# Optimization experiments

Measured on AMD Instinct MI355X. Metric: run time of the kernel, lower is better.

## Reference

```python
import jax, jax.numpy as jnp
import numpy as np

HEADS = 16
DIM_HEAD = 64
DIM = 1024
INNER = HEADS * DIM_HEAD  # 1024


def setup_inputs() -> dict:
    key = jax.random.key(0)
    ks = jax.random.split(key, 8)
    B, N, M = 4, 2048, 2048
    x = jax.random.normal(ks[0], (B, N, DIM), dtype=jnp.float32)
    context = jax.random.normal(ks[1], (B, M, DIM), dtype=jnp.float32)
    x_mask = (jax.random.uniform(ks[2], (B, N)) > 0.1).astype(jnp.float32)
    context_mask = (jax.random.uniform(ks[3], (B, M)) > 0.1).astype(jnp.float32)
    s = 0.02
    Wq = jax.random.normal(ks[4], (DIM, INNER), dtype=jnp.float32) * s
    Wkv = jax.random.normal(ks[5], (DIM, 2 * INNER), dtype=jnp.float32) * s
    Wo = jax.random.normal(ks[6], (INNER, DIM), dtype=jnp.float32) * s
    bo = jnp.zeros((DIM,), dtype=jnp.float32)
    return {"x": x, "context": context, "x_mask": x_mask,
            "context_mask": context_mask, "Wq": Wq, "Wkv": Wkv, "Wo": Wo, "bo": bo}


def _split_heads(t):
    b, n, _ = t.shape
    return t.reshape(b, n, HEADS, DIM_HEAD).transpose(0, 2, 1, 3)  # b h n d


def reference(x, context, x_mask, context_mask, Wq, Wkv, Wo, bo):
    scale = DIM_HEAD ** -0.5
    q = _split_heads(x @ Wq)                       # b h n d
    kv = context @ Wkv
    k = _split_heads(kv[..., :INNER])              # b h m d
    v = _split_heads(kv[..., INNER:])              # b h m d
    dots = jnp.einsum('bhnd,bhmd->bhnm', q, k) * scale
    # attn_bias = 1 - x_mask ⊗ context_mask; masked where isclose(attn_bias, 1)
    prod = x_mask[:, None, :, None] * context_mask[:, None, None, :]  # b 1 n m
    masked = jnp.isclose(1.0 - prod, 1.0)          # b 1 n m, broadcast over heads
    dots = jnp.where(masked, -jnp.inf, dots)       # b h n m
    # rows with no valid key: zero the whole row before softmax
    valid = jnp.any(~masked, axis=-1, keepdims=True)  # b 1 n 1
    dots = jnp.where(valid, dots, 0.0)
    attn = jax.nn.softmax(dots, axis=-1)
    attn = jnp.where(valid, attn, 0.0)
    out = jnp.einsum('bhnm,bhmd->bhnd', attn, v)
    b, h, n, d = out.shape
    out = out.transpose(0, 2, 1, 3).reshape(b, n, h * d)
    return out @ Wo + bo
```

## Files before the change

### kernel.cpp

```cpp
#include <hip/hip_runtime.h>

#define DEVI __device__ __forceinline__

typedef __attribute__((ext_vector_type(4))) float f32x4;
typedef __attribute__((ext_vector_type(8))) _Float16 f16x8;
typedef __attribute__((ext_vector_type(2))) _Float16 f16x2;
typedef __attribute__((ext_vector_type(4))) unsigned u32x4;

#if __has_builtin(__builtin_amdgcn_exp2f)
#define EXP2F __builtin_amdgcn_exp2f
#else
#define EXP2F exp2f
#endif

DEVI ushort f2h(float f) {
  _Float16 h = (_Float16)f;
  return __builtin_bit_cast(ushort, h);
}

DEVI unsigned pkrtz(float a, float b) {
  return __builtin_bit_cast(unsigned, __builtin_amdgcn_cvt_pkrtz(a, b));
}

DEVI float dot2acc(unsigned pk, float acc) {
#if __has_builtin(__builtin_amdgcn_fdot2)
  f16x2 one2 = {(_Float16)1.0f, (_Float16)1.0f};
  return __builtin_amdgcn_fdot2(__builtin_bit_cast(f16x2, pk), one2, acc, false);
#else
  f16x2 v = __builtin_bit_cast(f16x2, pk);
  return acc + (float)v[0] + (float)v[1];
#endif
}

DEVI void gload_lds16(const void* g, void* l) {
  typedef const unsigned int GlobU __attribute__((address_space(1)));
  typedef unsigned int LdsU __attribute__((address_space(3)));
  __builtin_amdgcn_global_load_lds((GlobU*)g, (LdsU*)l, 16, 0, 0);
}

__global__ __launch_bounds__(256) void cast_f16_kernel(
    const float4* __restrict__ x, const float4* __restrict__ ctx,
    ushort4* __restrict__ xo, ushort4* __restrict__ co) {
  int i = blockIdx.x * 256 + threadIdx.x;
  const float4* src;
  ushort4* dst;
  int j;
  if (i < 2097152) { src = x; dst = xo; j = i; }
  else             { src = ctx; dst = co; j = i - 2097152; }
  float4 v = src[j];
  ushort4 o;
  o.x = f2h(v.x); o.y = f2h(v.y); o.z = f2h(v.z); o.w = f2h(v.w);
  dst[j] = o;
}

__global__ __launch_bounds__(256) void transpose_cast_kernel(
    const float* __restrict__ Wq, const float* __restrict__ Wkv,
    const float* __restrict__ Wo, ushort* __restrict__ WqT,
    ushort* __restrict__ WkvT, ushort* __restrict__ WoT) {
  __shared__ ushort tile[64][65];
  int bx = blockIdx.x;
  const float* in; ushort* out; int C, cb;
  if (bx < 16)      { in = Wq;  out = WqT;  C = 1024; cb = bx * 64; }
  else if (bx < 48) { in = Wkv; out = WkvT; C = 2048; cb = (bx - 16) * 64; }
  else              { in = Wo;  out = WoT;  C = 1024; cb = (bx - 48) * 64; }
  const int R = 1024;
  int rb = blockIdx.y * 64;
  int t = threadIdx.x;
  int c4 = (t & 15) * 4, r0 = t >> 4;
#pragma unroll
  for (int i = 0; i < 4; i++) {
    int r = r0 + i * 16;
    float4 v = *(const float4*)(in + (size_t)(rb + r) * C + cb + c4);
    tile[r][c4 + 0] = f2h(v.x);
    tile[r][c4 + 1] = f2h(v.y);
    tile[r][c4 + 2] = f2h(v.z);
    tile[r][c4 + 3] = f2h(v.w);
  }
  __syncthreads();
#pragma unroll
  for (int i = 0; i < 4; i++) {
    int rr = r0 + i * 16;
    ushort4 o;
    o.x = tile[c4 + 0][rr]; o.y = tile[c4 + 1][rr];
    o.z = tile[c4 + 2][rr]; o.w = tile[c4 + 3][rr];
    *(ushort4*)(out + (size_t)(cb + rr) * R + rb + c4) = o;
  }
}

DEVI void gemm_stage(const ushort* __restrict__ A, const ushort* __restrict__ Bt,
                     int K, int rowbase, int colbase, int tid, int wave,
                     ushort* AsC, ushort* BsC, int kk) {
#pragma unroll
  for (int i = 0; i < 2; i++) {
    int f = i * 256 + tid;
    int r = f >> 2;
    int c = (f & 3) ^ (r & 3);
    gload_lds16(A + (size_t)(rowbase + r) * K + (kk + c * 8),
                (char*)AsC + (size_t)(i * 256 + wave * 64) * 16);
    gload_lds16(Bt + (size_t)(colbase + r) * K + (kk + c * 8),
                (char*)BsC + (size_t)(i * 256 + wave * 64) * 16);
  }
}

DEVI void gemm_core(const ushort* __restrict__ A, const ushort* __restrict__ Bt,
                    const int K, int rowbase, int colbase, int tid,
                    ushort* As, ushort* Bs, f32x4 acc[4][4]) {
  const int lane = tid & 63, wave = tid >> 6;
  const int quad = lane >> 4, ln = lane & 15;
  const int wrow = (wave >> 1) * 64, wcol = (wave & 1) * 64;

  gemm_stage(A, Bt, K, rowbase, colbase, tid, wave, As, Bs, 0);
  gemm_stage(A, Bt, K, rowbase, colbase, tid, wave, As + 4096, Bs + 4096, 32);

  for (int k0 = 0; k0 < K; k0 += 32) {
    const int cur = (k0 >> 5) & 1;
    ushort* AsC = As + cur * 4096;
    ushort* BsC = Bs + cur * 4096;

    if (k0 + 32 < K) asm volatile("s_waitcnt vmcnt(4)" ::: "memory");
    else             asm volatile("s_waitcnt vmcnt(0)" ::: "memory");
    asm volatile("s_barrier" ::: "memory");

    f16x8 a[4], b[4];
#pragma unroll
    for (int mt = 0; mt < 4; mt++) {
      int r = wrow + mt * 16 + ln;
      a[mt] = *(const f16x8*)(AsC + ((size_t)r * 4 + (quad ^ (r & 3))) * 8);
    }
#pragma unroll
    for (int nt = 0; nt < 4; nt++) {
      int r = wcol + nt * 16 + ln;
      b[nt] = *(const f16x8*)(BsC + ((size_t)r * 4 + (quad ^ (r & 3))) * 8);
    }
#pragma unroll
    for (int mt = 0; mt < 4; mt++)
#pragma unroll
      for (int nt = 0; nt < 4; nt++)
        acc[mt][nt] = __builtin_amdgcn_mfma_f32_16x16x32_f16(a[mt], b[nt], acc[mt][nt], 0, 0, 0);

    asm volatile("s_barrier" ::: "memory");
    if (k0 + 64 < K)
      gemm_stage(A, Bt, K, rowbase, colbase, tid, wave, AsC, BsC, k0 + 64);
  }
}

__global__ __launch_bounds__(256, 3) void qkv_gemm(
    const ushort* __restrict__ xb, const ushort* __restrict__ cb,
    const ushort* __restrict__ WqT, const ushort* __restrict__ WkvT,
    ushort* __restrict__ Qo, ushort* __restrict__ Ko, ushort* __restrict__ Vo) {
  __shared__ ushort As[2 * 128 * 32];
  __shared__ ushort Bs[2 * 128 * 32];
  const int tid = threadIdx.x;
  const int lane = tid & 63, wave = tid >> 6;
  const int quad = lane >> 4, ln = lane & 15;
  const int cy = blockIdx.y;
  const bool isQ = cy < 8;
  const int colbase = (isQ ? cy : cy - 8) * 128;
  const int rowbase = blockIdx.x * 128;
  const int wrow = (wave >> 1) * 64, wcol = (wave & 1) * 64;
  f32x4 acc[4][4] = {};
  gemm_core(isQ ? xb : cb, isQ ? WqT : WkvT, 1024, rowbase, colbase, tid, As, Bs, acc);

  if (isQ) {
    const float qs = 0.18033688011112042f;
#pragma unroll
    for (int nt = 0; nt < 4; nt++) {
      int col = colbase + wcol + nt * 16 + ln;
      int h = col >> 6, d = col & 63;
#pragma unroll
      for (int mt = 0; mt < 4; mt++) {
        int row = rowbase + wrow + mt * 16 + quad * 4;
        int bb = row >> 11, n = row & 2047;
        uint2 pv;
        pv.x = pkrtz(acc[mt][nt][0] * qs, acc[mt][nt][1] * qs);
        pv.y = pkrtz(acc[mt][nt][2] * qs, acc[mt][nt][3] * qs);
        *(uint2*)(Qo + (((size_t)bb * 16 + h) * 64 + d) * 2048 + n) = pv;
      }
    }
  } else {
    bool isK = (colbase < 1024);
#pragma unroll
    for (int nt = 0; nt < 4; nt++) {
      int col = colbase + wcol + nt * 16 + ln;
#pragma unroll
      for (int mt = 0; mt < 4; mt++) {
        int row = rowbase + wrow + mt * 16 + quad * 4;
        int bb = row >> 11, m = row & 2047;
        if (isK) {
          int h = col >> 6, d = col & 63;
#pragma unroll
          for (int r = 0; r < 4; r++)
            Ko[(((size_t)bb * 16 + h) * 2048 + (m + r)) * 64 + d] = f2h(acc[mt][nt][r]);
        } else {
          int c2 = col - 1024;
          int h = c2 >> 6, d = c2 & 63;
          uint2 pv;
          pv.x = pkrtz(acc[mt][nt][0], acc[mt][nt][1]);
          pv.y = pkrtz(acc[mt][nt][2], acc[mt][nt][3]);
          *(uint2*)(Vo + (((size_t)bb * 16 + h) * 64 + d) * 2048 + m) = pv;
        }
      }
    }
  }
}

__global__ __launch_bounds__(256, 3) void out_gemm(
    const ushort* __restrict__ A, const ushort* __restrict__ Bt,
    float* __restrict__ C, const float* __restrict__ bias) {
  __shared__ ushort As[2 * 128 * 32];
  __shared__ ushort Bs[2 * 128 * 32];
  const int tid = threadIdx.x;
  const int lane = tid & 63, wave = tid >> 6;
  const int quad = lane >> 4, ln = lane & 15;
  const int colbase = blockIdx.y * 128, rowbase = blockIdx.x * 128;
  const int wrow = (wave >> 1) * 64, wcol = (wave & 1) * 64;
  f32x4 acc[4][4] = {};
  gemm_core(A, Bt, 1024, rowbase, colbase, tid, As, Bs, acc);
#pragma unroll
  for (int nt = 0; nt < 4; nt++) {
    int col = colbase + wcol + nt * 16 + ln;
    float bv = bias[col];
#pragma unroll
    for (int mt = 0; mt < 4; mt++) {
      int row = rowbase + wrow + mt * 16 + quad * 4;
#pragma unroll
      for (int r = 0; r < 4; r++)
        C[(size_t)(row + r) * 1024 + col] = acc[mt][nt][r] + bv;
    }
  }
}

__global__ __launch_bounds__(256, 2) void attn_kernel(
    const ushort* __restrict__ QT, const ushort* __restrict__ K,
    const ushort* __restrict__ VT, const float* __restrict__ xmask,
    const float* __restrict__ cmask, ushort* __restrict__ O) {
  __shared__ ushort Ks[2][64 * 64];
  __shared__ ushort Vs[2][64 * 64];
  __shared__ float CMB[2048];
  const int tid = threadIdx.x, lane = tid & 63, wave = tid >> 6;
  const int quad = lane >> 4, ln = lane & 15;
  const int bid = blockIdx.x;
  const int qb = bid >> 6, bh6 = bid & 63, h = bh6 & 15, b = bh6 >> 4;
  const size_t bh = (size_t)b * 16 + h;
  const ushort* QTbh = QT + bh * (64 * 2048);
  const ushort* Kbh = K + bh * (2048 * 64);
  const ushort* Vbh = VT + bh * (64 * 2048);
  const int q0 = qb * 256 + wave * 64;

  {
#pragma unroll
    for (int i = 0; i < 2; i++) {
      float4 c0 = *(const float4*)(cmask + b * 2048 + tid * 8 + i * 4);
      float4 b0;
      b0.x = fmaf(c0.x, 3.0e4f, -3.0e4f); b0.y = fmaf(c0.y, 3.0e4f, -3.0e4f);
      b0.z = fmaf(c0.z, 3.0e4f, -3.0e4f); b0.w = fmaf(c0.w, 3.0e4f, -3.0e4f);
      *(float4*)(CMB + tid * 8 + i * 4) = b0;
    }
  }

  f16x8 qf[4][2];
#pragma unroll
  for (int qt = 0; qt < 4; qt++)
#pragma unroll
    for (int kc = 0; kc < 2; kc++) {
      int q = q0 + qt * 16 + ln;
#pragma unroll
      for (int j = 0; j < 8; j++)
        qf[qt][kc][j] = __builtin_bit_cast(_Float16,
            (unsigned short)QTbh[(size_t)(kc * 32 + quad * 8 + j) * 2048 + q]);
    }

  float xm[4];
#pragma unroll
  for (int qt = 0; qt < 4; qt++) xm[qt] = xmask[b * 2048 + q0 + qt * 16 + ln];

  __syncthreads();

#pragma unroll
  for (int t = 0; t < 2; t++) {
#pragma unroll
    for (int i = 0; i < 2; i++) {
      int f = i * 256 + tid;
      int r = f >> 3;
      int c = (f & 7) ^ (r & 7);
      int rp = (r & 32) | ((r & 12) << 1) | ((r & 16) >> 2) | (r & 3);
      gload_lds16(Kbh + (size_t)(t * 64 + rp) * 64 + c * 8, (char*)Ks[t] + (size_t)f * 16);
      gload_lds16(Vbh + (size_t)r * 2048 + (t * 64 + c * 8), (char*)Vs[t] + (size_t)f * 16);
    }
  }

  f32x4 o[4][4] = {};
  float lpart[4] = {0.f, 0.f, 0.f, 0.f};

  for (int kb = 0; kb < 32; kb++) {
    const int cur = kb & 1;
    const int m0 = kb * 64;
    const ushort* KsC = Ks[cur];
    const ushort* VsC = Vs[cur];

    if (kb < 31) asm volatile("s_waitcnt vmcnt(4)" ::: "memory");
    else         asm volatile("s_waitcnt vmcnt(0)" ::: "memory");
    asm volatile("s_barrier" ::: "memory");

    f32x4 bias4[4];
#pragma unroll
    for (int kt = 0; kt < 4; kt++)
      bias4[kt] = *(const f32x4*)(CMB + m0 + (kt >> 1) * 32 + quad * 8 + (kt & 1) * 4);

    f32x4 s[4][4];
#pragma unroll
    for (int kt = 0; kt < 4; kt++)
#pragma unroll
      for (int qt = 0; qt < 4; qt++) s[kt][qt] = bias4[kt];
#pragma unroll
    for (int kc = 0; kc < 2; kc++) {
#pragma unroll
      for (int kt = 0; kt < 4; kt++) {
        int r = kt * 16 + ln;
        f16x8 ka = *(const f16x8*)(KsC + ((size_t)r * 8 + ((kc * 4 + quad) ^ (r & 7))) * 8);
#pragma unroll
        for (int qt = 0; qt < 4; qt++)
          s[kt][qt] = __builtin_amdgcn_mfma_f32_16x16x32_f16(ka, qf[qt][kc], s[kt][qt], 0, 0, 0);
      }
    }

#pragma unroll
    for (int kc = 0; kc < 2; kc++) {
      f16x8 pf[4];
#pragma unroll
      for (int qt = 0; qt < 4; qt++) {
        f32x4 sA = s[kc * 2 + 0][qt];
        f32x4 sB = s[kc * 2 + 1][qt];
        u32x4 u;
        u[0] = pkrtz(EXP2F(sA[0]), EXP2F(sA[1]));
        u[1] = pkrtz(EXP2F(sA[2]), EXP2F(sA[3]));
        u[2] = pkrtz(EXP2F(sB[0]), EXP2F(sB[1]));
        u[3] = pkrtz(EXP2F(sB[2]), EXP2F(sB[3]));
        lpart[qt] = dot2acc(u[0], lpart[qt]);
        lpart[qt] = dot2acc(u[1], lpart[qt]);
        lpart[qt] = dot2acc(u[2], lpart[qt]);
        lpart[qt] = dot2acc(u[3], lpart[qt]);
        pf[qt] = __builtin_bit_cast(f16x8, u);
      }
#pragma unroll
      for (int dt = 0; dt < 4; dt++) {
        int r = dt * 16 + ln;
        f16x8 va = *(const f16x8*)(VsC + ((size_t)r * 8 + ((kc * 4 + quad) ^ (r & 7))) * 8);
#pragma unroll
        for (int qt = 0; qt < 4; qt++)
          o[dt][qt] = __builtin_amdgcn_mfma_f32_16x16x32_f16(va, pf[qt], o[dt][qt], 0, 0, 0);
      }
    }

    asm volatile("s_barrier" ::: "memory");
    if (kb < 30) {
      const int m2 = m0 + 128;
#pragma unroll
      for (int i = 0; i < 2; i++) {
        int f = i * 256 + tid;
        int r = f >> 3;
        int c = (f & 7) ^ (r & 7);
        int rp = (r & 32) | ((r & 12) << 1) | ((r & 16) >> 2) | (r & 3);
        gload_lds16(Kbh + (size_t)(m2 + rp) * 64 + c * 8, (char*)Ks[cur] + (size_t)f * 16);
        gload_lds16(Vbh + (size_t)r * 2048 + (m2 + c * 8), (char*)Vs[cur] + (size_t)f * 16);
      }
    }
  }

#pragma unroll
  for (int qt = 0; qt < 4; qt++) {
    float l = lpart[qt];
    l += __shfl_xor(l, 16, 64);
    l += __shfl_xor(l, 32, 64);
    float inv = (xm[qt] != 0.f && l > 0.f) ? (1.f / l) : 0.f;
    int n = q0 + qt * 16 + ln;
    ushort* ob = O + ((size_t)(b * 2048 + n) * 16 + h) * 64;
#pragma unroll
    for (int dt = 0; dt < 4; dt++) {
      uint2 pv;
      pv.x = pkrtz(o[dt][qt][0] * inv, o[dt][qt][1] * inv);
      pv.y = pkrtz(o[dt][qt][2] * inv, o[dt][qt][3] * inv);
      *(uint2*)(ob + dt * 16 + quad * 4) = pv;
    }
  }
}

extern "C" void kernel_launch(void* const* d_in, const int* in_sizes, int n_in,
                              void* d_out, int out_size, void* d_ws, size_t ws_size,
                              hipStream_t stream) {
  const float* x   = (const float*)d_in[0];
  const float* ctx = (const float*)d_in[1];
  const float* xm  = (const float*)d_in[2];
  const float* cm  = (const float*)d_in[3];
  const float* Wq  = (const float*)d_in[4];
  const float* Wkv = (const float*)d_in[5];
  const float* Wo  = (const float*)d_in[6];
  const float* bo  = (const float*)d_in[7];

  char* ws = (char*)d_ws;
  const size_t MB = 1024 * 1024;
  ushort* xb   = (ushort*)(ws + 0);
  ushort* cb   = (ushort*)(ws + 16 * MB);
  ushort* WqT  = (ushort*)(ws + 32 * MB);
  ushort* WkvT = (ushort*)(ws + 34 * MB);
  ushort* WoT  = (ushort*)(ws + 38 * MB);
  ushort* QTb  = (ushort*)(ws + 40 * MB);
  ushort* Kb   = (ushort*)(ws + 56 * MB);
  ushort* VTb  = (ushort*)(ws + 72 * MB);
  ushort* Ob   = xb;

  cast_f16_kernel<<<16384, 256, 0, stream>>>((const float4*)x, (const float4*)ctx,
                                             (ushort4*)xb, (ushort4*)cb);
  transpose_cast_kernel<<<dim3(64, 16), 256, 0, stream>>>(Wq, Wkv, Wo, WqT, WkvT, WoT);
  qkv_gemm<<<dim3(64, 24), 256, 0, stream>>>(xb, cb, WqT, WkvT, QTb, Kb, VTb);
  attn_kernel<<<512, 256, 0, stream>>>(QTb, Kb, VTb, xm, cm, Ob);
  out_gemm<<<dim3(64, 8), 256, 0, stream>>>(Ob, WoT, (float*)d_out, bo);
}
```

Measured before the change: 297.2 us.

## Split attention key range across two wave groups and merge partial outputs

```diff
diff --git a/kernel.cpp b/kernel.cpp
--- a/kernel.cpp
+++ b/kernel.cpp
@@ -230,32 +230,31 @@
   }
 }
 
-__global__ __launch_bounds__(256, 2) void attn_kernel(
+__global__ __launch_bounds__(512, 4) void attn_kernel(
     const ushort* __restrict__ QT, const ushort* __restrict__ K,
     const ushort* __restrict__ VT, const float* __restrict__ xmask,
     const float* __restrict__ cmask, ushort* __restrict__ O) {
-  __shared__ ushort Ks[2][64 * 64];
-  __shared__ ushort Vs[2][64 * 64];
+  __shared__ ushort SM[32768];
   __shared__ float CMB[2048];
+  ushort* KsB = SM;
+  ushort* VsB = SM + 16384;
   const int tid = threadIdx.x, lane = tid & 63, wave = tid >> 6;
   const int quad = lane >> 4, ln = lane & 15;
+  const int qw = wave & 3, hf = wave >> 2;
   const int bid = blockIdx.x;
   const int qb = bid >> 6, bh6 = bid & 63, h = bh6 & 15, b = bh6 >> 4;
   const size_t bh = (size_t)b * 16 + h;
   const ushort* QTbh = QT + bh * (64 * 2048);
   const ushort* Kbh = K + bh * (2048 * 64);
   const ushort* Vbh = VT + bh * (64 * 2048);
-  const int q0 = qb * 256 + wave * 64;
+  const int q0 = qb * 256 + qw * 64;
 
   {
-#pragma unroll
-    for (int i = 0; i < 2; i++) {
-      float4 c0 = *(const float4*)(cmask + b * 2048 + tid * 8 + i * 4);
-      float4 b0;
-      b0.x = fmaf(c0.x, 3.0e4f, -3.0e4f); b0.y = fmaf(c0.y, 3.0e4f, -3.0e4f);
-      b0.z = fmaf(c0.z, 3.0e4f, -3.0e4f); b0.w = fmaf(c0.w, 3.0e4f, -3.0e4f);
-      *(float4*)(CMB + tid * 8 + i * 4) = b0;
-    }
+    float4 c0 = *(const float4*)(cmask + b * 2048 + tid * 4);
+    float4 b0;
+    b0.x = fmaf(c0.x, 3.0e4f, -3.0e4f); b0.y = fmaf(c0.y, 3.0e4f, -3.0e4f);
+    b0.z = fmaf(c0.z, 3.0e4f, -3.0e4f); b0.w = fmaf(c0.w, 3.0e4f, -3.0e4f);
+    *(float4*)(CMB + tid * 4) = b0;
   }
 
   f16x8 qf[4][2];
@@ -276,30 +275,33 @@
 
   __syncthreads();
 
-#pragma unroll
-  for (int t = 0; t < 2; t++) {
-#pragma unroll
-    for (int i = 0; i < 2; i++) {
-      int f = i * 256 + tid;
-      int r = f >> 3;
-      int c = (f & 7) ^ (r & 7);
-      int rp = (r & 32) | ((r & 12) << 1) | ((r & 16) >> 2) | (r & 3);
-      gload_lds16(Kbh + (size_t)(t * 64 + rp) * 64 + c * 8, (char*)Ks[t] + (size_t)f * 16);
-      gload_lds16(Vbh + (size_t)r * 2048 + (t * 64 + c * 8), (char*)Vs[t] + (size_t)f * 16);
+  const int sr = tid >> 3;
+  const int sc = (tid & 7) ^ (sr & 7);
+  const int srp = (sr & 32) | ((sr & 12) << 1) | ((sr & 16) >> 2) | (sr & 3);
+
+#pragma unroll
+  for (int p = 0; p < 2; p++) {
+#pragma unroll
+    for (int f = 0; f < 2; f++) {
+      int m0 = f * 1024 + p * 64;
+      gload_lds16(Kbh + (size_t)(m0 + srp) * 64 + sc * 8,
+                  (char*)(KsB + (f * 2 + p) * 4096) + (size_t)tid * 16);
+      gload_lds16(Vbh + (size_t)sr * 2048 + (m0 + sc * 8),
+                  (char*)(VsB + (f * 2 + p) * 4096) + (size_t)tid * 16);
     }
   }
 
   f32x4 o[4][4] = {};
   float lpart[4] = {0.f, 0.f, 0.f, 0.f};
 
-  for (int kb = 0; kb < 32; kb++) {
-    const int cur = kb & 1;
-    const int m0 = kb * 64;
-    const ushort* KsC = Ks[cur];
-    const ushort* VsC = Vs[cur];
-
-    if (kb < 31) asm volatile("s_waitcnt vmcnt(4)" ::: "memory");
-    else         asm volatile("s_waitcnt vmcnt(0)" ::: "memory");
+  for (int p = 0; p < 16; p++) {
+    const int cur = p & 1;
+    const int m0 = hf * 1024 + p * 64;
+    const ushort* KsC = KsB + (hf * 2 + cur) * 4096;
+    const ushort* VsC = VsB + (hf * 2 + cur) * 4096;
+
+    if (p < 15) asm volatile("s_waitcnt vmcnt(4)" ::: "memory");
+    else        asm volatile("s_waitcnt vmcnt(0)" ::: "memory");
     asm volatile("s_barrier" ::: "memory");
 
     f32x4 bias4[4];
@@ -353,34 +355,57 @@
     }
 
     asm volatile("s_barrier" ::: "memory");
-    if (kb < 30) {
-      const int m2 = m0 + 128;
-#pragma unroll
-      for (int i = 0; i < 2; i++) {
-        int f = i * 256 + tid;
-        int r = f >> 3;
-        int c = (f & 7) ^ (r & 7);
-        int rp = (r & 32) | ((r & 12) << 1) | ((r & 16) >> 2) | (r & 3);
-        gload_lds16(Kbh + (size_t)(m2 + rp) * 64 + c * 8, (char*)Ks[cur] + (size_t)f * 16);
-        gload_lds16(Vbh + (size_t)r * 2048 + (m2 + c * 8), (char*)Vs[cur] + (size_t)f * 16);
-      }
-    }
-  }
-
-#pragma unroll
-  for (int qt = 0; qt < 4; qt++) {
-    float l = lpart[qt];
-    l += __shfl_xor(l, 16, 64);
-    l += __shfl_xor(l, 32, 64);
-    float inv = (xm[qt] != 0.f && l > 0.f) ? (1.f / l) : 0.f;
-    int n = q0 + qt * 16 + ln;
-    ushort* ob = O + ((size_t)(b * 2048 + n) * 16 + h) * 64;
-#pragma unroll
-    for (int dt = 0; dt < 4; dt++) {
-      uint2 pv;
-      pv.x = pkrtz(o[dt][qt][0] * inv, o[dt][qt][1] * inv);
-      pv.y = pkrtz(o[dt][qt][2] * inv, o[dt][qt][3] * inv);
-      *(uint2*)(ob + dt * 16 + quad * 4) = pv;
+    if (p < 14) {
+      const int p2 = p + 2;
+#pragma unroll
+      for (int f = 0; f < 2; f++) {
+        int mm = f * 1024 + p2 * 64;
+        gload_lds16(Kbh + (size_t)(mm + srp) * 64 + sc * 8,
+                    (char*)(KsB + (f * 2 + cur) * 4096) + (size_t)tid * 16);
+        gload_lds16(Vbh + (size_t)sr * 2048 + (mm + sc * 8),
+                    (char*)(VsB + (f * 2 + cur) * 4096) + (size_t)tid * 16);
+      }
+    }
+  }
+
+  __syncthreads();
+  if (wave >= 4) {
+    f32x4* mrg = (f32x4*)SM;
+    int w4 = wave - 4;
+#pragma unroll
+    for (int dt = 0; dt < 4; dt++)
+#pragma unroll
+      for (int qt = 0; qt < 4; qt++)
+        mrg[(size_t)((w4 * 16 + dt * 4 + qt) * 64) + lane] = o[dt][qt];
+#pragma unroll
+    for (int qt = 0; qt < 4; qt++) CMB[(wave * 4 + qt - 16) * 64 + lane] = lpart[qt];
+  }
+  __syncthreads();
+  if (wave < 4) {
+    f32x4* mrg = (f32x4*)SM;
+#pragma unroll
+    for (int dt = 0; dt < 4; dt++)
+#pragma unroll
+      for (int qt = 0; qt < 4; qt++)
+        o[dt][qt] += mrg[(size_t)((wave * 16 + dt * 4 + qt) * 64) + lane];
+#pragma unroll
+    for (int qt = 0; qt < 4; qt++) lpart[qt] += CMB[(wave * 4 + qt) * 64 + lane];
+
+#pragma unroll
+    for (int qt = 0; qt < 4; qt++) {
+      float l = lpart[qt];
+      l += __shfl_xor(l, 16, 64);
+      l += __shfl_xor(l, 32, 64);
+      float inv = (xm[qt] != 0.f && l > 0.f) ? (1.f / l) : 0.f;
+      int n = q0 + qt * 16 + ln;
+      ushort* ob = O + ((size_t)(b * 2048 + n) * 16 + h) * 64;
+#pragma unroll
+      for (int dt = 0; dt < 4; dt++) {
+        uint2 pv;
+        pv.x = pkrtz(o[dt][qt][0] * inv, o[dt][qt][1] * inv);
+        pv.y = pkrtz(o[dt][qt][2] * inv, o[dt][qt][3] * inv);
+        *(uint2*)(ob + dt * 16 + quad * 4) = pv;
+      }
     }
   }
 }
@@ -413,6 +438,6 @@
                                              (ushort4*)xb, (ushort4*)cb);
   transpose_cast_kernel<<<dim3(64, 16), 256, 0, stream>>>(Wq, Wkv, Wo, WqT, WkvT, WoT);
   qkv_gemm<<<dim3(64, 24), 256, 0, stream>>>(xb, cb, WqT, WkvT, QTb, Kb, VTb);
-  attn_kernel<<<512, 256, 0, stream>>>(QTb, Kb, VTb, xm, cm, Ob);
+  attn_kernel<<<512, 512, 0, stream>>>(QTb, Kb, VTb, xm, cm, Ob);
   out_gemm<<<dim3(64, 8), 256, 0, stream>>>(Ob, WoT, (float*)d_out, bo);
 }
```

Measured after the change: 634.9 us. 114% more time.

## Software-pipeline QK of next tile with softmax/PV of current tile

Applied to the files above, without the earlier changes.

```diff
diff --git a/kernel.cpp b/kernel.cpp
--- a/kernel.cpp
+++ b/kernel.cpp
@@ -234,9 +234,11 @@
     const ushort* __restrict__ QT, const ushort* __restrict__ K,
     const ushort* __restrict__ VT, const float* __restrict__ xmask,
     const float* __restrict__ cmask, ushort* __restrict__ O) {
-  __shared__ ushort Ks[2][64 * 64];
+  __shared__ ushort Ks[3][64 * 64];
   __shared__ ushort Vs[2][64 * 64];
   __shared__ float CMB[2048];
+  char* KsBase = (char*)Ks;
+  char* VsBase = (char*)Vs;
   const int tid = threadIdx.x, lane = tid & 63, wave = tid >> 6;
   const int quad = lane >> 4, ln = lane & 15;
   const int bid = blockIdx.x;
@@ -247,15 +249,13 @@
   const ushort* Vbh = VT + bh * (64 * 2048);
   const int q0 = qb * 256 + wave * 64;
 
-  {
-#pragma unroll
-    for (int i = 0; i < 2; i++) {
-      float4 c0 = *(const float4*)(cmask + b * 2048 + tid * 8 + i * 4);
-      float4 b0;
-      b0.x = fmaf(c0.x, 3.0e4f, -3.0e4f); b0.y = fmaf(c0.y, 3.0e4f, -3.0e4f);
-      b0.z = fmaf(c0.z, 3.0e4f, -3.0e4f); b0.w = fmaf(c0.w, 3.0e4f, -3.0e4f);
-      *(float4*)(CMB + tid * 8 + i * 4) = b0;
-    }
+#pragma unroll
+  for (int i = 0; i < 2; i++) {
+    float4 c0 = *(const float4*)(cmask + b * 2048 + tid * 8 + i * 4);
+    float4 b0;
+    b0.x = fmaf(c0.x, 3.0e4f, -3.0e4f); b0.y = fmaf(c0.y, 3.0e4f, -3.0e4f);
+    b0.z = fmaf(c0.z, 3.0e4f, -3.0e4f); b0.w = fmaf(c0.w, 3.0e4f, -3.0e4f);
+    *(float4*)(CMB + tid * 8 + i * 4) = b0;
   }
 
   f16x8 qf[4][2];
@@ -276,95 +276,122 @@
 
   __syncthreads();
 
-#pragma unroll
-  for (int t = 0; t < 2; t++) {
+  auto STAGE_K = [&](int t, int off) {
 #pragma unroll
     for (int i = 0; i < 2; i++) {
       int f = i * 256 + tid;
-      int r = f >> 3;
-      int c = (f & 7) ^ (r & 7);
+      int r = f >> 3, c = (f & 7) ^ (r & 7);
       int rp = (r & 32) | ((r & 12) << 1) | ((r & 16) >> 2) | (r & 3);
-      gload_lds16(Kbh + (size_t)(t * 64 + rp) * 64 + c * 8, (char*)Ks[t] + (size_t)f * 16);
-      gload_lds16(Vbh + (size_t)r * 2048 + (t * 64 + c * 8), (char*)Vs[t] + (size_t)f * 16);
-    }
-  }
+      gload_lds16(Kbh + (size_t)(t * 64 + rp) * 64 + c * 8,
+                  KsBase + off + (size_t)f * 16);
+    }
+  };
+  auto STAGE_V = [&](int t, int off) {
+#pragma unroll
+    for (int i = 0; i < 2; i++) {
+      int f = i * 256 + tid;
+      int r = f >> 3, c = (f & 7) ^ (r & 7);
+      gload_lds16(Vbh + (size_t)r * 2048 + (t * 64 + c * 8),
+                  VsBase + off + (size_t)f * 16);
+    }
+  };
+
+  STAGE_K(0, 0); STAGE_V(0, 0); STAGE_K(1, 8192); STAGE_V(1, 8192); STAGE_K(2, 16384);
 
   f32x4 o[4][4] = {};
   float lpart[4] = {0.f, 0.f, 0.f, 0.f};
-
-  for (int kb = 0; kb < 32; kb++) {
-    const int cur = kb & 1;
-    const int m0 = kb * 64;
-    const ushort* KsC = Ks[cur];
-    const ushort* VsC = Vs[cur];
-
-    if (kb < 31) asm volatile("s_waitcnt vmcnt(4)" ::: "memory");
-    else         asm volatile("s_waitcnt vmcnt(0)" ::: "memory");
-    asm volatile("s_barrier" ::: "memory");
-
-    f32x4 bias4[4];
-#pragma unroll
-    for (int kt = 0; kt < 4; kt++)
-      bias4[kt] = *(const f32x4*)(CMB + m0 + (kt >> 1) * 32 + quad * 8 + (kt & 1) * 4);
-
-    f32x4 s[4][4];
-#pragma unroll
-    for (int kt = 0; kt < 4; kt++)
-#pragma unroll
-      for (int qt = 0; qt < 4; qt++) s[kt][qt] = bias4[kt];
-#pragma unroll
-    for (int kc = 0; kc < 2; kc++) {
-#pragma unroll
-      for (int kt = 0; kt < 4; kt++) {
-        int r = kt * 16 + ln;
-        f16x8 ka = *(const f16x8*)(KsC + ((size_t)r * 8 + ((kc * 4 + quad) ^ (r & 7))) * 8);
-#pragma unroll
-        for (int qt = 0; qt < 4; qt++)
-          s[kt][qt] = __builtin_amdgcn_mfma_f32_16x16x32_f16(ka, qf[qt][kc], s[kt][qt], 0, 0, 0);
-      }
-    }
-
-#pragma unroll
-    for (int kc = 0; kc < 2; kc++) {
-      f16x8 pf[4];
-#pragma unroll
-      for (int qt = 0; qt < 4; qt++) {
-        f32x4 sA = s[kc * 2 + 0][qt];
-        f32x4 sB = s[kc * 2 + 1][qt];
-        u32x4 u;
-        u[0] = pkrtz(EXP2F(sA[0]), EXP2F(sA[1]));
-        u[1] = pkrtz(EXP2F(sA[2]), EXP2F(sA[3]));
-        u[2] = pkrtz(EXP2F(sB[0]), EXP2F(sB[1]));
-        u[3] = pkrtz(EXP2F(sB[2]), EXP2F(sB[3]));
-        lpart[qt] = dot2acc(u[0], lpart[qt]);
-        lpart[qt] = dot2acc(u[1], lpart[qt]);
-        lpart[qt] = dot2acc(u[2], lpart[qt]);
-        lpart[qt] = dot2acc(u[3], lpart[qt]);
-        pf[qt] = __builtin_bit_cast(f16x8, u);
-      }
-#pragma unroll
-      for (int dt = 0; dt < 4; dt++) {
-        int r = dt * 16 + ln;
-        f16x8 va = *(const f16x8*)(VsC + ((size_t)r * 8 + ((kc * 4 + quad) ^ (r & 7))) * 8);
-#pragma unroll
-        for (int qt = 0; qt < 4; qt++)
-          o[dt][qt] = __builtin_amdgcn_mfma_f32_16x16x32_f16(va, pf[qt], o[dt][qt], 0, 0, 0);
-      }
-    }
-
-    asm volatile("s_barrier" ::: "memory");
-    if (kb < 30) {
-      const int m2 = m0 + 128;
-#pragma unroll
-      for (int i = 0; i < 2; i++) {
-        int f = i * 256 + tid;
-        int r = f >> 3;
-        int c = (f & 7) ^ (r & 7);
-        int rp = (r & 32) | ((r & 12) << 1) | ((r & 16) >> 2) | (r & 3);
-        gload_lds16(Kbh + (size_t)(m2 + rp) * 64 + c * 8, (char*)Ks[cur] + (size_t)f * 16);
-        gload_lds16(Vbh + (size_t)r * 2048 + (m2 + c * 8), (char*)Vs[cur] + (size_t)f * 16);
-      }
-    }
+  f32x4 sEa[2][4], sEb[2][4];
+  int kO0 = 0, kO1 = 8192, kO2 = 16384;
+
+#define QK_EARLY(KsPtr, mOff, sOUT) do {                                          \
+    f32x4 b0_ = *(const f32x4*)(CMB + (mOff) + quad * 8);                         \
+    f32x4 b1_ = *(const f32x4*)(CMB + (mOff) + quad * 8 + 4);                     \
+    _Pragma("unroll") for (int kt_ = 0; kt_ < 2; kt_++) {                         \
+      int r_ = kt_ * 16 + ln;                                                     \
+      f16x8 ka_ = *(const f16x8*)((KsPtr) + ((size_t)r_ * 8 + (quad ^ (r_ & 7))) * 8); \
+      _Pragma("unroll") for (int qt_ = 0; qt_ < 4; qt_++)                         \
+        sOUT[kt_][qt_] = __builtin_amdgcn_mfma_f32_16x16x32_f16(                  \
+            ka_, qf[qt_][0], kt_ ? b1_ : b0_, 0, 0, 0);                           \
+    }                                                                             \
+    _Pragma("unroll") for (int kt_ = 0; kt_ < 2; kt_++) {                         \
+      int r_ = kt_ * 16 + ln;                                                     \
+      f16x8 ka_ = *(const f16x8*)((KsPtr) + ((size_t)r_ * 8 + ((4 + quad) ^ (r_ & 7))) * 8); \
+      _Pragma("unroll") for (int qt_ = 0; qt_ < 4; qt_++)                         \
+        sOUT[kt_][qt_] = __builtin_amdgcn_mfma_f32_16x16x32_f16(                  \
+            ka_, qf[qt_][1], sOUT[kt_][qt_], 0, 0, 0);                            \
+    }                                                                             \
+  } while (0)
+
+#define QK_LATE(KsPtr, mOff, sOUT) do {                                           \
+    f32x4 b2_ = *(const f32x4*)(CMB + (mOff) + 32 + quad * 8);                    \
+    f32x4 b3_ = *(const f32x4*)(CMB + (mOff) + 32 + quad * 8 + 4);                \
+    _Pragma("unroll") for (int kt_ = 0; kt_ < 2; kt_++) {                         \
+      int r_ = (kt_ + 2) * 16 + ln;                                               \
+      f16x8 ka_ = *(const f16x8*)((KsPtr) + ((size_t)r_ * 8 + (quad ^ (r_ & 7))) * 8); \
+      _Pragma("unroll") for (int qt_ = 0; qt_ < 4; qt_++)                         \
+        sOUT[kt_][qt_] = __builtin_amdgcn_mfma_f32_16x16x32_f16(                  \
+            ka_, qf[qt_][0], kt_ ? b3_ : b2_, 0, 0, 0);                           \
+    }                                                                             \
+    _Pragma("unroll") for (int kt_ = 0; kt_ < 2; kt_++) {                         \
+      int r_ = (kt_ + 2) * 16 + ln;                                               \
+      f16x8 ka_ = *(const f16x8*)((KsPtr) + ((size_t)r_ * 8 + ((4 + quad) ^ (r_ & 7))) * 8); \
+      _Pragma("unroll") for (int qt_ = 0; qt_ < 4; qt_++)                         \
+        sOUT[kt_][qt_] = __builtin_amdgcn_mfma_f32_16x16x32_f16(                  \
+            ka_, qf[qt_][1], sOUT[kt_][qt_], 0, 0, 0);                            \
+    }                                                                             \
+  } while (0)
+
+#define SM_PV(sX, vkc, VsC_) do {                                                 \
+    f16x8 pf_[4];                                                                 \
+    _Pragma("unroll") for (int qt_ = 0; qt_ < 4; qt_++) {                         \
+      u32x4 u_;                                                                   \
+      u_[0] = pkrtz(EXP2F(sX[0][qt_][0]), EXP2F(sX[0][qt_][1]));                  \
+      u_[1] = pkrtz(EXP2F(sX[0][qt_][2]), EXP2F(sX[0][qt_][3]));                  \
+      u_[2] = pkrtz(EXP2F(sX[1][qt_][0]), EXP2F(sX[1][qt_][1]));                  \
+      u_[3] = pkrtz(EXP2F(sX[1][qt_][2]), EXP2F(sX[1][qt_][3]));                  \
+      lpart[qt_] = dot2acc(u_[0], lpart[qt_]);                                    \
+      lpart[qt_] = dot2acc(u_[1], lpart[qt_]);                                    \
+      lpart[qt_] = dot2acc(u_[2], lpart[qt_]);                                    \
+      lpart[qt_] = dot2acc(u_[3], lpart[qt_]);                                    \
+      pf_[qt_] = __builtin_bit_cast(f16x8, u_);                                   \
+    }                                                                             \
+    _Pragma("unroll") for (int dt_ = 0; dt_ < 4; dt_++) {                         \
+      int r_ = dt_ * 16 + ln;                                                     \
+      f16x8 va_ = *(const f16x8*)((VsC_) + ((size_t)r_ * 8 + (((vkc) + quad) ^ (r_ & 7))) * 8); \
+      _Pragma("unroll") for (int qt_ = 0; qt_ < 4; qt_++)                         \
+        o[dt_][qt_] = __builtin_amdgcn_mfma_f32_16x16x32_f16(va_, pf_[qt_], o[dt_][qt_], 0, 0, 0); \
+    }                                                                             \
+  } while (0)
+
+#define PHASE(p, sIN, sOUT) do {                                                  \
+    if ((p) < 30)       asm volatile("s_waitcnt vmcnt(4)" ::: "memory");          \
+    else if ((p) == 30) asm volatile("s_waitcnt vmcnt(2)" ::: "memory");          \
+    else                asm volatile("s_waitcnt vmcnt(0)" ::: "memory");          \
+    asm volatile("s_barrier" ::: "memory");                                       \
+    const ushort* KsC_ = (const ushort*)(KsBase + kO0);                           \
+    const ushort* VsC_ = (const ushort*)(VsBase + ((p) & 1) * 8192);              \
+    const int m0_ = (p) * 64;                                                     \
+    f32x4 sL[2][4];                                                               \
+    QK_LATE(KsC_, m0_, sL);                                                       \
+    SM_PV(sIN, 0, VsC_);                                                          \
+    if ((p) < 31) {                                                               \
+      const ushort* KsN_ = (const ushort*)(KsBase + kO1);                         \
+      QK_EARLY(KsN_, m0_ + 64, sOUT);                                             \
+    }                                                                             \
+    SM_PV(sL, 4, VsC_);                                                           \
+    asm volatile("s_barrier" ::: "memory");                                       \
+    if ((p) < 29) STAGE_K((p) + 3, kO0);                                          \
+    if ((p) < 30) STAGE_V((p) + 2, ((p) & 1) * 8192);                             \
+    { int tt_ = kO0; kO0 = kO1; kO1 = kO2; kO2 = tt_; }                           \
+  } while (0)
+
+  asm volatile("s_waitcnt vmcnt(8)" ::: "memory");
+  asm volatile("s_barrier" ::: "memory");
+  QK_EARLY((const ushort*)KsBase, 0, sEa);
+
+  for (int pp = 0; pp < 16; pp++) {
+    PHASE(2 * pp, sEa, sEb);
+    PHASE(2 * pp + 1, sEb, sEa);
   }
 
 #pragma unroll
@@ -383,6 +410,10 @@
       *(uint2*)(ob + dt * 16 + quad * 4) = pv;
     }
   }
+#undef PHASE
+#undef SM_PV
+#undef QK_LATE
+#undef QK_EARLY
 }
 
 extern "C" void kernel_launch(void* const* d_in, const int* in_sizes, int n_in,
```

After: 304.7 us. 1.03x slower.

## Load K/V fragments directly from global into registers, drop LDS staging

Applied to the files above, without the earlier changes.

```diff
diff --git a/kernel.cpp b/kernel.cpp
--- a/kernel.cpp
+++ b/kernel.cpp
@@ -234,8 +234,6 @@
     const ushort* __restrict__ QT, const ushort* __restrict__ K,
     const ushort* __restrict__ VT, const float* __restrict__ xmask,
     const float* __restrict__ cmask, ushort* __restrict__ O) {
-  __shared__ ushort Ks[2][64 * 64];
-  __shared__ ushort Vs[2][64 * 64];
   __shared__ float CMB[2048];
   const int tid = threadIdx.x, lane = tid & 63, wave = tid >> 6;
   const int quad = lane >> 4, ln = lane & 15;
@@ -247,15 +245,13 @@
   const ushort* Vbh = VT + bh * (64 * 2048);
   const int q0 = qb * 256 + wave * 64;
 
-  {
-#pragma unroll
-    for (int i = 0; i < 2; i++) {
-      float4 c0 = *(const float4*)(cmask + b * 2048 + tid * 8 + i * 4);
-      float4 b0;
-      b0.x = fmaf(c0.x, 3.0e4f, -3.0e4f); b0.y = fmaf(c0.y, 3.0e4f, -3.0e4f);
-      b0.z = fmaf(c0.z, 3.0e4f, -3.0e4f); b0.w = fmaf(c0.w, 3.0e4f, -3.0e4f);
-      *(float4*)(CMB + tid * 8 + i * 4) = b0;
-    }
+#pragma unroll
+  for (int i = 0; i < 2; i++) {
+    float4 c0 = *(const float4*)(cmask + b * 2048 + tid * 8 + i * 4);
+    float4 b0;
+    b0.x = fmaf(c0.x, 3.0e4f, -3.0e4f); b0.y = fmaf(c0.y, 3.0e4f, -3.0e4f);
+    b0.z = fmaf(c0.z, 3.0e4f, -3.0e4f); b0.w = fmaf(c0.w, 3.0e4f, -3.0e4f);
+    *(float4*)(CMB + tid * 8 + i * 4) = b0;
   }
 
   f16x8 qf[4][2];
@@ -276,31 +272,28 @@
 
   __syncthreads();
 
-#pragma unroll
-  for (int t = 0; t < 2; t++) {
-#pragma unroll
-    for (int i = 0; i < 2; i++) {
-      int f = i * 256 + tid;
-      int r = f >> 3;
-      int c = (f & 7) ^ (r & 7);
-      int rp = (r & 32) | ((r & 12) << 1) | ((r & 16) >> 2) | (r & 3);
-      gload_lds16(Kbh + (size_t)(t * 64 + rp) * 64 + c * 8, (char*)Ks[t] + (size_t)f * 16);
-      gload_lds16(Vbh + (size_t)r * 2048 + (t * 64 + c * 8), (char*)Vs[t] + (size_t)f * 16);
-    }
-  }
+  const ushort* kpL = Kbh + (size_t)((ln >> 2) * 8 + (ln & 3)) * 64 + quad * 8;
+  const ushort* vpL = Vbh + (size_t)ln * 2048 + quad * 8;
 
   f32x4 o[4][4] = {};
   float lpart[4] = {0.f, 0.f, 0.f, 0.f};
 
-  for (int kb = 0; kb < 32; kb++) {
-    const int cur = kb & 1;
-    const int m0 = kb * 64;
-    const ushort* KsC = Ks[cur];
-    const ushort* VsC = Vs[cur];
-
-    if (kb < 31) asm volatile("s_waitcnt vmcnt(4)" ::: "memory");
-    else         asm volatile("s_waitcnt vmcnt(0)" ::: "memory");
-    asm volatile("s_barrier" ::: "memory");
+  for (int p = 0; p < 32; p++) {
+    const int m0 = p * 64;
+
+    f16x8 kf[2][4];
+#pragma unroll
+    for (int kc = 0; kc < 2; kc++)
+#pragma unroll
+      for (int kt = 0; kt < 4; kt++)
+        kf[kc][kt] = *(const f16x8*)(kpL + (size_t)m0 * 64 +
+                                     ((kt >> 1) * 32 + (kt & 1) * 4) * 64 + kc * 32);
+    f16x8 vf[2][4];
+#pragma unroll
+    for (int kc = 0; kc < 2; kc++)
+#pragma unroll
+      for (int dt = 0; dt < 4; dt++)
+        vf[kc][dt] = *(const f16x8*)(vpL + (size_t)dt * 32768 + m0 + kc * 32);
 
     f32x4 bias4[4];
 #pragma unroll
@@ -311,18 +304,13 @@
 #pragma unroll
     for (int kt = 0; kt < 4; kt++)
 #pragma unroll
-      for (int qt = 0; qt < 4; qt++) s[kt][qt] = bias4[kt];
-#pragma unroll
-    for (int kc = 0; kc < 2; kc++) {
-#pragma unroll
-      for (int kt = 0; kt < 4; kt++) {
-        int r = kt * 16 + ln;
-        f16x8 ka = *(const f16x8*)(KsC + ((size_t)r * 8 + ((kc * 4 + quad) ^ (r & 7))) * 8);
-#pragma unroll
-        for (int qt = 0; qt < 4; qt++)
-          s[kt][qt] = __builtin_amdgcn_mfma_f32_16x16x32_f16(ka, qf[qt][kc], s[kt][qt], 0, 0, 0);
-      }
-    }
+      for (int qt = 0; qt < 4; qt++)
+        s[kt][qt] = __builtin_amdgcn_mfma_f32_16x16x32_f16(kf[0][kt], qf[qt][0], bias4[kt], 0, 0, 0);
+#pragma unroll
+    for (int kt = 0; kt < 4; kt++)
+#pragma unroll
+      for (int qt = 0; qt < 4; qt++)
+        s[kt][qt] = __builtin_amdgcn_mfma_f32_16x16x32_f16(kf[1][kt], qf[qt][1], s[kt][qt], 0, 0, 0);
 
 #pragma unroll
     for (int kc = 0; kc < 2; kc++) {
@@ -343,27 +331,10 @@
         pf[qt] = __builtin_bit_cast(f16x8, u);
       }
 #pragma unroll
-      for (int dt = 0; dt < 4; dt++) {
-        int r = dt * 16 + ln;
-        f16x8 va = *(const f16x8*)(VsC + ((size_t)r * 8 + ((kc * 4 + quad) ^ (r & 7))) * 8);
+      for (int dt = 0; dt < 4; dt++)
 #pragma unroll
         for (int qt = 0; qt < 4; qt++)
-          o[dt][qt] = __builtin_amdgcn_mfma_f32_16x16x32_f16(va, pf[qt], o[dt][qt], 0, 0, 0);
-      }
-    }
-
-    asm volatile("s_barrier" ::: "memory");
-    if (kb < 30) {
-      const int m2 = m0 + 128;
-#pragma unroll
-      for (int i = 0; i < 2; i++) {
-        int f = i * 256 + tid;
-        int r = f >> 3;
-        int c = (f & 7) ^ (r & 7);
-        int rp = (r & 32) | ((r & 12) << 1) | ((r & 16) >> 2) | (r & 3);
-        gload_lds16(Kbh + (size_t)(m2 + rp) * 64 + c * 8, (char*)Ks[cur] + (size_t)f * 16);
-        gload_lds16(Vbh + (size_t)r * 2048 + (m2 + c * 8), (char*)Vs[cur] + (size_t)f * 16);
-      }
+          o[dt][qt] = __builtin_amdgcn_mfma_f32_16x16x32_f16(vf[kc][dt], pf[qt], o[dt][qt], 0, 0, 0);
     }
   }
 
```

Result: slower. 351.8 us (+18.3%).
